# Kernel optimization log

Hardware: AMD Instinct MI355X
Metric: run time of the kernel (lower is better)

Reference implementation:

```python
import jax, jax.numpy as jnp
import numpy as np

B, T, C, H = 4, 2048, 1024, 16
NEG = -1e9  # masked-fill value (finite to keep grads clean)


def setup_inputs() -> dict:
    key = jax.random.key(0)
    ks = jax.random.split(key, 5)
    s = 1.0 / np.sqrt(C)  # keep logits O(1) like trained linear layers
    return {
        "x": jax.random.normal(ks[0], (B, T, C), dtype=jnp.float32),
        "wq": jax.random.normal(ks[1], (C, C), dtype=jnp.float32) * s,
        "bq": jnp.zeros((C,), dtype=jnp.float32),
        "wk": jax.random.normal(ks[2], (C, C), dtype=jnp.float32) * s,
        "bk": jnp.zeros((C,), dtype=jnp.float32),
        "wv": jax.random.normal(ks[3], (C, C), dtype=jnp.float32) * s,
        "bv": jnp.zeros((C,), dtype=jnp.float32),
        "wo": jax.random.normal(ks[4], (C, C), dtype=jnp.float32) * s,
        "bo": jnp.zeros((C,), dtype=jnp.float32),
    }


def _split_heads(y):
    # [B,T,C] -> [B,H,T,hd]
    b, t, c = y.shape
    return y.reshape(b, t, H, c // H).transpose(0, 2, 1, 3)


def reference(x, wq, bq, wk, bk, wv, bv, wo, bo):
    b, t, c = x.shape
    scale = (c // H) ** (-0.5)
    q = _split_heads(x @ wq.T + bq)  # [B,H,T,hd]
    k = _split_heads(x @ wk.T + bk)
    v = _split_heads(x @ wv.T + bv)
    att = jnp.einsum("bhqd,bhkd->bhqk", q, k) * scale  # [B,H,T,T]
    causal = jnp.tril(jnp.ones((t, t), dtype=bool))
    att = jnp.where(causal[None, None], att, NEG)
    att = jax.nn.softmax(att, axis=-1)  # dropout is identity in eval mode
    y = jnp.einsum("bhqk,bhkd->bhqd", att, v)
    y = y.transpose(0, 2, 1, 3).reshape(b, t, c)
    return y @ wo.T + bo
```

## Files before the change

### kernel.cpp

```cpp
#include <hip/hip_runtime.h>


#define B_ 4
#define T_ 2048
#define C_ 1024
#define H_ 16
#define M_ 8192

typedef unsigned short u16;
typedef __bf16 bf16x8 __attribute__((ext_vector_type(8)));
typedef float f32x4 __attribute__((ext_vector_type(4)));

static __device__ __forceinline__ u16 f2bf(float f) {
  unsigned int u = __float_as_uint(f);
  u += 0x7fffu + ((u >> 16) & 1u);
  return (u16)(u >> 16);
}

static __device__ __forceinline__ void async16(const void* g, void* l) {
  __builtin_amdgcn_global_load_lds(
      (const __attribute__((address_space(1))) unsigned int*)g,
      (__attribute__((address_space(3))) unsigned int*)l, 16, 0, 0);
}

#if __has_builtin(__builtin_amdgcn_exp2f)
#define EXP2F(x) __builtin_amdgcn_exp2f(x)
#else
#define EXP2F(x) exp2f(x)
#endif

static __device__ __forceinline__ f32x4 mfma32(bf16x8 a, bf16x8 b, f32x4 c) {
  return __builtin_amdgcn_mfma_f32_16x16x32_bf16(a, b, c, 0, 0, 0);
}

#define FENCE() asm volatile("" ::: "memory")

__global__ __launch_bounds__(256) void cvt_all(const float* __restrict__ x,
                                               const float* __restrict__ w0,
                                               const float* __restrict__ w1,
                                               const float* __restrict__ w2,
                                               const float* __restrict__ w3,
                                               u16* __restrict__ xb,
                                               u16* __restrict__ wb,
                                               float s0) {
  const int NX = M_ * C_ / 4, NW = C_ * C_ / 4;
  int i = blockIdx.x * 256 + threadIdx.x;
  const float* src;
  u16* dst;
  int idx;
  float s = 1.f;
  if (i < NX) {
    src = x; dst = xb; idx = i;
  } else {
    int j = i - NX;
    int w = j / NW;
    idx = j - w * NW;
    src = (w == 0) ? w0 : (w == 1) ? w1 : (w == 2) ? w2 : w3;
    dst = wb + (size_t)w * C_ * C_;
    if (w == 0) s = s0;
  }
  float4 f = ((const float4*)src)[idx];
  ushort4 o;
  o.x = f2bf(f.x * s); o.y = f2bf(f.y * s); o.z = f2bf(f.z * s); o.w = f2bf(f.w * s);
  ((ushort4*)dst)[idx] = o;
}

__global__ __launch_bounds__(512, 2) void gemm_qkv(const u16* __restrict__ A,
                                                   const u16* __restrict__ W,
                                                   const float* __restrict__ bq,
                                                   const float* __restrict__ bk,
                                                   const float* __restrict__ bv,
                                                   float qscale,
                                                   u16* __restrict__ outqk,
                                                   u16* __restrict__ vtb) {
  __shared__ __align__(16) union {
    u16 buf[3][24576];
    u16 Cu[256 * 136];
    u16 Ct[128 * 272];
  } sm;
  const int tid = threadIdx.x, lane = tid & 63, wave = tid >> 6;
  const int quad = lane >> 4, l16 = lane & 15;
  const int wm = wave >> 1, wn = wave & 1;
  const int bid = blockIdx.x;
  const int xcd = bid & 7, idx = bid >> 3;
  const int cq = idx >> 2;
  const int row0 = (xcd * 4 + (idx & 3)) * 256;
  const int sel = cq >> 3, colw = cq & 7;
  const int col0 = colw * 128;
  const u16* Bt = W + (size_t)sel * C_ * C_;
  const float* bias = sel == 0 ? bq : (sel == 1 ? bk : bv);
  const float bscale = sel == 0 ? qscale : 1.f;

  const u16* aptr[4];
  const u16* bptr[2];
#pragma unroll
  for (int it = 0; it < 4; it++) {
    int c = it * 512 + tid, r = c >> 3, g = (c & 7) ^ (r & 7);
    aptr[it] = A + (size_t)(row0 + r) * C_ + g * 8;
  }
#pragma unroll
  for (int it = 0; it < 2; it++) {
    int c = it * 512 + tid, r = c >> 3, g = (c & 7) ^ (r & 7);
    bptr[it] = Bt + (size_t)(col0 + r) * C_ + g * 8;
  }

  auto STAGE = [&](int t, int pp) {
    const int k0 = t * 64;
    u16* lA = sm.buf[pp];
    u16* lB = sm.buf[pp] + 16384;
#pragma unroll
    for (int it = 0; it < 4; it++)
      async16(aptr[it] + k0, lA + (size_t)(it * 512 + wave * 64) * 8);
#pragma unroll
    for (int it = 0; it < 2; it++)
      async16(bptr[it] + k0, lB + (size_t)(it * 512 + wave * 64) * 8);
  };

  f32x4 zero = {0.f, 0.f, 0.f, 0.f};
  f32x4 acc[4][4];
#pragma unroll
  for (int i = 0; i < 4; i++)
#pragma unroll
    for (int j = 0; j < 4; j++) acc[i][j] = zero;

  STAGE(0, 0);
  STAGE(1, 1);

  int p = 0, p2 = 2;
#pragma unroll 1
  for (int u = 0; u < 16; ++u) {
    FENCE();
    __builtin_amdgcn_s_barrier();
    FENCE();
    if (u < 14) STAGE(u + 2, p2);
    if (u < 14) {
      asm volatile("s_waitcnt vmcnt(12)" ::: "memory");
    } else if (u < 15) {
      asm volatile("s_waitcnt vmcnt(6)" ::: "memory");
    } else {
      asm volatile("s_waitcnt vmcnt(0)" ::: "memory");
    }
    FENCE();
    __builtin_amdgcn_s_barrier();
    FENCE();

    const u16* As = sm.buf[p];
    const u16* Bs = sm.buf[p] + 16384;
    bf16x8 bfr[4][2];
#pragma unroll
    for (int j = 0; j < 4; j++) {
      int rn = wn * 64 + 16 * j + l16;
#pragma unroll
      for (int kk = 0; kk < 2; kk++)
        bfr[j][kk] =
            *(const bf16x8*)(Bs + rn * 64 + (((kk * 4 + quad) ^ (rn & 7)) * 8));
    }
    {
      bf16x8 a2[2][2];
#pragma unroll
      for (int i = 0; i < 2; i++) {
        int rm = wm * 64 + 16 * i + l16;
#pragma unroll
        for (int kk = 0; kk < 2; kk++)
          a2[i][kk] =
              *(const bf16x8*)(As + rm * 64 + (((kk * 4 + quad) ^ (rm & 7)) * 8));
      }
      __builtin_amdgcn_s_setprio(1);
#pragma unroll
      for (int i = 0; i < 2; i++)
#pragma unroll
        for (int j = 0; j < 4; j++) {
          acc[i][j] = mfma32(a2[i][0], bfr[j][0], acc[i][j]);
          acc[i][j] = mfma32(a2[i][1], bfr[j][1], acc[i][j]);
        }
      __builtin_amdgcn_s_setprio(0);
    }
    FENCE();
    __builtin_amdgcn_s_barrier();
    FENCE();
    {
      bf16x8 a2[2][2];
#pragma unroll
      for (int i = 0; i < 2; i++) {
        int rm = wm * 64 + 16 * (i + 2) + l16;
#pragma unroll
        for (int kk = 0; kk < 2; kk++)
          a2[i][kk] =
              *(const bf16x8*)(As + rm * 64 + (((kk * 4 + quad) ^ (rm & 7)) * 8));
      }
      __builtin_amdgcn_s_setprio(1);
#pragma unroll
      for (int i = 0; i < 2; i++)
#pragma unroll
        for (int j = 0; j < 4; j++) {
          acc[i + 2][j] = mfma32(a2[i][0], bfr[j][0], acc[i + 2][j]);
          acc[i + 2][j] = mfma32(a2[i][1], bfr[j][1], acc[i + 2][j]);
        }
      __builtin_amdgcn_s_setprio(0);
    }
    asm volatile("s_waitcnt lgkmcnt(0)" ::: "memory");
    p = (p == 2) ? 0 : p + 1;
    p2 = (p2 == 2) ? 0 : p2 + 1;
  }
  __syncthreads();

  float bj[4];
#pragma unroll
  for (int j = 0; j < 4; j++) bj[j] = bias[col0 + wn * 64 + 16 * j + l16] * bscale;

  if (sel == 2) {
#pragma unroll
    for (int i = 0; i < 4; i++)
#pragma unroll
      for (int j = 0; j < 4; j++) {
        int lc = wn * 64 + 16 * j + l16;
        int rt = wm * 64 + 16 * i + quad * 4;
        union { u16 s[4]; uint2 u; } w;
#pragma unroll
        for (int r = 0; r < 4; r++) w.s[r] = f2bf(acc[i][j][r] + bj[j]);
        *(uint2*)(sm.Ct + (size_t)lc * 272 + rt) = w.u;
      }
    __syncthreads();
    const int bb = row0 >> 11, t0 = row0 & 2047;
#pragma unroll
    for (int c2 = 0; c2 < 8; c2++) {
      int c = c2 * 512 + tid;
      int nr = c >> 5, ch = c & 31;
      bf16x8 v = *(const bf16x8*)(sm.Ct + (size_t)nr * 272 + ch * 8);
      int gn = col0 + nr, d = gn & 63, hh = gn >> 6;
      *(bf16x8*)(vtb + ((size_t)((bb * 16 + hh) * 64 + d)) * T_ + t0 + ch * 8) = v;
    }
  } else {
#pragma unroll
    for (int i = 0; i < 4; i++)
#pragma unroll
      for (int j = 0; j < 4; j++) {
        int lc = wn * 64 + 16 * j + l16;
        int rt = wm * 64 + 16 * i + quad * 4;
#pragma unroll
        for (int r = 0; r < 4; r++)
          sm.Cu[(size_t)(rt + r) * 136 + lc] = f2bf(acc[i][j][r] + bj[j]);
      }
    __syncthreads();
    u16* dst = outqk + (size_t)sel * M_ * C_;
#pragma unroll
    for (int c2 = 0; c2 < 8; c2++) {
      int c = c2 * 512 + tid;
      int rw = c >> 4, ch = c & 15;
      bf16x8 v = *(const bf16x8*)(sm.Cu + (size_t)rw * 136 + ch * 8);
      *(bf16x8*)(dst + (size_t)(row0 + rw) * C_ + col0 + ch * 8) = v;
    }
  }
}

__global__ __launch_bounds__(512, 2) void gemm_o(const u16* __restrict__ A,
                                                 const u16* __restrict__ Bt,
                                                 const float* __restrict__ bias,
                                                 float* __restrict__ outf) {
  __shared__ __align__(16) union {
    u16 buf[3][24576];
    float Cf[256 * 132];
  } sm;
  const int tid = threadIdx.x, lane = tid & 63, wave = tid >> 6;
  const int quad = lane >> 4, l16 = lane & 15;
  const int wm = wave >> 1, wn = wave & 1;
  const int bid = blockIdx.x;
  const int xcd = bid & 7, idx = bid >> 3;
  const int row0 = (xcd * 4 + (idx & 3)) * 256;
  const int col0 = (idx >> 2) * 128;

  const u16* aptr[4];
  const u16* bptr[2];
#pragma unroll
  for (int it = 0; it < 4; it++) {
    int c = it * 512 + tid, r = c >> 3, g = (c & 7) ^ (r & 7);
    aptr[it] = A + (size_t)(row0 + r) * C_ + g * 8;
  }
#pragma unroll
  for (int it = 0; it < 2; it++) {
    int c = it * 512 + tid, r = c >> 3, g = (c & 7) ^ (r & 7);
    bptr[it] = Bt + (size_t)(col0 + r) * C_ + g * 8;
  }

  auto STAGE = [&](int t, int pp) {
    const int k0 = t * 64;
    u16* lA = sm.buf[pp];
    u16* lB = sm.buf[pp] + 16384;
#pragma unroll
    for (int it = 0; it < 4; it++)
      async16(aptr[it] + k0, lA + (size_t)(it * 512 + wave * 64) * 8);
#pragma unroll
    for (int it = 0; it < 2; it++)
      async16(bptr[it] + k0, lB + (size_t)(it * 512 + wave * 64) * 8);
  };

  f32x4 zero = {0.f, 0.f, 0.f, 0.f};
  f32x4 acc[4][4];
#pragma unroll
  for (int i = 0; i < 4; i++)
#pragma unroll
    for (int j = 0; j < 4; j++) acc[i][j] = zero;

  STAGE(0, 0);
  STAGE(1, 1);

  int p = 0, p2 = 2;
#pragma unroll 1
  for (int u = 0; u < 16; ++u) {
    FENCE();
    __builtin_amdgcn_s_barrier();
    FENCE();
    if (u < 14) STAGE(u + 2, p2);
    if (u < 14) {
      asm volatile("s_waitcnt vmcnt(12)" ::: "memory");
    } else if (u < 15) {
      asm volatile("s_waitcnt vmcnt(6)" ::: "memory");
    } else {
      asm volatile("s_waitcnt vmcnt(0)" ::: "memory");
    }
    FENCE();
    __builtin_amdgcn_s_barrier();
    FENCE();

    const u16* As = sm.buf[p];
    const u16* Bs = sm.buf[p] + 16384;
    bf16x8 bfr[4][2];
#pragma unroll
    for (int j = 0; j < 4; j++) {
      int rn = wn * 64 + 16 * j + l16;
#pragma unroll
      for (int kk = 0; kk < 2; kk++)
        bfr[j][kk] =
            *(const bf16x8*)(Bs + rn * 64 + (((kk * 4 + quad) ^ (rn & 7)) * 8));
    }
    {
      bf16x8 a2[2][2];
#pragma unroll
      for (int i = 0; i < 2; i++) {
        int rm = wm * 64 + 16 * i + l16;
#pragma unroll
        for (int kk = 0; kk < 2; kk++)
          a2[i][kk] =
              *(const bf16x8*)(As + rm * 64 + (((kk * 4 + quad) ^ (rm & 7)) * 8));
      }
      __builtin_amdgcn_s_setprio(1);
#pragma unroll
      for (int i = 0; i < 2; i++)
#pragma unroll
        for (int j = 0; j < 4; j++) {
          acc[i][j] = mfma32(a2[i][0], bfr[j][0], acc[i][j]);
          acc[i][j] = mfma32(a2[i][1], bfr[j][1], acc[i][j]);
        }
      __builtin_amdgcn_s_setprio(0);
    }
    FENCE();
    __builtin_amdgcn_s_barrier();
    FENCE();
    {
      bf16x8 a2[2][2];
#pragma unroll
      for (int i = 0; i < 2; i++) {
        int rm = wm * 64 + 16 * (i + 2) + l16;
#pragma unroll
        for (int kk = 0; kk < 2; kk++)
          a2[i][kk] =
              *(const bf16x8*)(As + rm * 64 + (((kk * 4 + quad) ^ (rm & 7)) * 8));
      }
      __builtin_amdgcn_s_setprio(1);
#pragma unroll
      for (int i = 0; i < 2; i++)
#pragma unroll
        for (int j = 0; j < 4; j++) {
          acc[i + 2][j] = mfma32(a2[i][0], bfr[j][0], acc[i + 2][j]);
          acc[i + 2][j] = mfma32(a2[i][1], bfr[j][1], acc[i + 2][j]);
        }
      __builtin_amdgcn_s_setprio(0);
    }
    asm volatile("s_waitcnt lgkmcnt(0)" ::: "memory");
    p = (p == 2) ? 0 : p + 1;
    p2 = (p2 == 2) ? 0 : p2 + 1;
  }
  __syncthreads();

  float bj[4];
#pragma unroll
  for (int j = 0; j < 4; j++) bj[j] = bias[col0 + wn * 64 + 16 * j + l16];

#pragma unroll
  for (int i = 0; i < 4; i++)
#pragma unroll
    for (int j = 0; j < 4; j++) {
      int lc = wn * 64 + 16 * j + l16;
      int rt = wm * 64 + 16 * i + quad * 4;
#pragma unroll
      for (int r = 0; r < 4; r++)
        sm.Cf[(size_t)(rt + r) * 132 + lc] = acc[i][j][r] + bj[j];
    }
  __syncthreads();
#pragma unroll
  for (int c2 = 0; c2 < 16; c2++) {
    int c = c2 * 512 + tid;
    int rw = c >> 5, c4 = c & 31;
    float4 v = *(const float4*)(sm.Cf + (size_t)rw * 132 + c4 * 4);
    *(float4*)(outf + (size_t)(row0 + rw) * C_ + col0 + c4 * 4) = v;
  }
}

__global__ __launch_bounds__(256) void attn(const u16* __restrict__ q,
                                            const u16* __restrict__ k,
                                            const u16* __restrict__ vt,
                                            u16* __restrict__ y) {
  __shared__ __align__(16) u16 Ksm[128 * 64];
  __shared__ __align__(16) u16 Vsm[2][64 * 64];
  __shared__ __align__(16) u16 Psm[4][32 * 64];
  const int tid = threadIdx.x, lane = tid & 63, wave = tid >> 6;
  const int quad = lane >> 4, l16 = lane & 15;
  static const int qperm[16] = {15, 14, 11, 10, 12, 13, 8, 9, 3, 2, 7, 6, 0, 1, 4, 5};
  const int bh = blockIdx.x;
  const int qt = qperm[blockIdx.y];
  const int b = bh >> 4, h = bh & 15;

  bf16x8 qf[2][2];
#pragma unroll
  for (int m = 0; m < 2; m++) {
    const u16* qp =
        q + (size_t)(b * T_ + qt * 128 + wave * 32 + m * 16 + l16) * C_ + h * 64;
#pragma unroll
    for (int ks = 0; ks < 2; ks++)
      qf[m][ks] = *(const bf16x8*)(qp + ks * 32 + quad * 8);
  }

  f32x4 zero = {0.f, 0.f, 0.f, 0.f};
  f32x4 o[2][4];
  float lp[2][4];
#pragma unroll
  for (int m = 0; m < 2; m++) {
#pragma unroll
    for (int dt = 0; dt < 4; dt++) o[m][dt] = zero;
#pragma unroll
    for (int r = 0; r < 4; r++) lp[m][r] = 0.f;
  }

  const u16* kp[4];
  const u16* vp[4];
#pragma unroll
  for (int i = 0; i < 4; i++) {
    int c = i * 256 + tid;
    int r = c >> 3, lc = (c & 7) ^ (r & 7);
    kp[i] = k + (size_t)(b * T_ + r) * C_ + h * 64 + lc * 8;
  }
#pragma unroll
  for (int s = 0; s < 2; s++)
#pragma unroll
    for (int i = 0; i < 2; i++) {
      int c = i * 256 + tid;
      int r = c >> 3, lc = (c & 7) ^ (r & 7);
      vp[s * 2 + i] = vt + (size_t)(bh * 64 + r) * T_ + 64 * s + lc * 8;
    }

  int qrel[2];
#pragma unroll
  for (int m = 0; m < 2; m++)
    qrel[m] = wave * 32 + m * 16 + quad * 4 - l16;

  u16* Pw = &Psm[wave][0];

#pragma unroll 1
  for (int jt = 0; jt <= qt; ++jt) {
#pragma unroll
    for (int i = 0; i < 4; i++) {
      async16(kp[i], Ksm + (size_t)(i * 256 + wave * 64) * 8);
      kp[i] += (size_t)128 * C_;
    }
#pragma unroll
    for (int s = 0; s < 2; s++)
#pragma unroll
      for (int i = 0; i < 2; i++) {
        async16(vp[s * 2 + i], Vsm[s] + (size_t)(i * 256 + wave * 64) * 8);
        vp[s * 2 + i] += 128;
      }
    __syncthreads();

    const bool diag = (jt == qt);
#pragma unroll
    for (int hh = 0; hh < 2; ++hh) {
      if (diag && (2 * wave + 2 - 4 * hh) <= 0) continue;
#pragma unroll
      for (int n = 0; n < 4; ++n) {
        int rk = hh * 64 + n * 16 + l16;
        bf16x8 kf0 = *(const bf16x8*)(Ksm + rk * 64 + ((quad ^ (rk & 7)) * 8));
        bf16x8 kf1 = *(const bf16x8*)(Ksm + rk * 64 + (((4 + quad) ^ (rk & 7)) * 8));
#pragma unroll
        for (int m = 0; m < 2; ++m) {
          int nlim = diag ? (2 * wave + m + 1 - 4 * hh) : 4;
          if (n < nlim) {
            f32x4 s = mfma32(qf[m][0], kf0, zero);
            s = mfma32(qf[m][1], kf1, s);
            float e[4];
#pragma unroll
            for (int r = 0; r < 4; r++) e[r] = EXP2F(s[r]);
            if (diag) {
              int rmin = hh * 64 + n * 16 - qrel[m];
#pragma unroll
              for (int r = 0; r < 4; r++)
                if (r < rmin) e[r] = 0.f;
            }
#pragma unroll
            for (int r = 0; r < 4; r++) {
              lp[m][r] += e[r];
              int qr = m * 16 + quad * 4 + r;
              Pw[qr * 64 + (((n * 2 + (l16 >> 3)) ^ (qr & 7)) * 8) + (l16 & 7)] =
                  f2bf(e[r]);
            }
          } else {
#pragma unroll
            for (int r = 0; r < 4; r++) {
              int qr = m * 16 + quad * 4 + r;
              Pw[qr * 64 + (((n * 2 + (l16 >> 3)) ^ (qr & 7)) * 8) + (l16 & 7)] = 0;
            }
          }
        }
      }
      bf16x8 pf[2][2];
#pragma unroll
      for (int m = 0; m < 2; m++)
#pragma unroll
        for (int ks = 0; ks < 2; ks++)
          pf[m][ks] = *(const bf16x8*)(Pw + (m * 16 + l16) * 64 +
                                       (((ks * 4 + quad) ^ (l16 & 7)) * 8));
#pragma unroll
      for (int dt = 0; dt < 4; ++dt) {
        int rv = dt * 16 + l16;
        bf16x8 vf0 = *(const bf16x8*)(Vsm[hh] + rv * 64 + ((quad ^ (rv & 7)) * 8));
        bf16x8 vf1 = *(const bf16x8*)(Vsm[hh] + rv * 64 + (((4 + quad) ^ (rv & 7)) * 8));
#pragma unroll
        for (int m = 0; m < 2; m++) {
          o[m][dt] = mfma32(pf[m][0], vf0, o[m][dt]);
          o[m][dt] = mfma32(pf[m][1], vf1, o[m][dt]);
        }
      }
    }
    __syncthreads();
  }

#pragma unroll
  for (int m = 0; m < 2; m++)
#pragma unroll
    for (int r = 0; r < 4; r++) {
      float v = lp[m][r];
      v += __shfl_xor(v, 1);
      v += __shfl_xor(v, 2);
      v += __shfl_xor(v, 4);
      v += __shfl_xor(v, 8);
      lp[m][r] = 1.f / v;
    }

#pragma unroll
  for (int m = 0; m < 2; m++)
#pragma unroll
    for (int r = 0; r < 4; r++) {
      int grow = b * T_ + qt * 128 + wave * 32 + m * 16 + quad * 4 + r;
#pragma unroll
      for (int dt = 0; dt < 4; dt++)
        y[(size_t)grow * C_ + h * 64 + dt * 16 + l16] = f2bf(o[m][dt][r] * lp[m][r]);
    }
}

extern "C" void kernel_launch(void* const* d_in, const int* in_sizes, int n_in,
                              void* d_out, int out_size, void* d_ws, size_t ws_size,
                              hipStream_t stream) {
  const float* x  = (const float*)d_in[0];
  const float* wq = (const float*)d_in[1];
  const float* bq = (const float*)d_in[2];
  const float* wk = (const float*)d_in[3];
  const float* bk = (const float*)d_in[4];
  const float* wv = (const float*)d_in[5];
  const float* bv = (const float*)d_in[6];
  const float* wo = (const float*)d_in[7];
  const float* bo = (const float*)d_in[8];
  float* out = (float*)d_out;

  const float QSCALE = 0.125f * 1.4426950408889634f;

  u16* xb  = (u16*)d_ws;
  u16* wqb = xb  + (size_t)M_ * C_;
  u16* wob = wqb + 3 * (size_t)C_ * C_;
  u16* qb  = wob + (size_t)C_ * C_;
  u16* kb  = qb  + (size_t)M_ * C_;
  u16* vtb = kb  + (size_t)M_ * C_;
  u16* yb  = xb;

  const int NCVT = (M_ * C_ + 4 * C_ * C_) / 4 / 256;
  cvt_all<<<NCVT, 256, 0, stream>>>(x, wq, wk, wv, wo, xb, wqb, QSCALE);

  gemm_qkv<<<768, 512, 0, stream>>>(xb, wqb, bq, bk, bv, QSCALE, qb, vtb);

  attn<<<dim3(B_ * H_, 16), 256, 0, stream>>>(qb, kb, vtb, yb);

  gemm_o<<<256, 512, 0, stream>>>(yb, wob, bo, out);
}
```

Before: 263.1 us.

## Transpose QK^T MFMA output in attention for vectorized P stores and cheaper row sums

Swaps the MFMA operand order so each lane holds four consecutive key columns of one query row. P can then be written to LDS as a single 4-element bf16 vector instead of four scalar stores, and row sums are kept per lane and reduced with two shuffles instead of sixteen. The causal mask condition is reworked to match the new orientation, and the final normalizer is gathered per row with a shuffle. Launch bounds for both GEMM kernels also drop from 2 to 1 blocks per CU, which frees registers but may reduce occupancy.

New measurement: 256.0 us. 1.03x faster.

```diff
diff --git a/kernel.cpp b/kernel.cpp
--- a/kernel.cpp
+++ b/kernel.cpp
@@ -9,6 +9,7 @@
 
 typedef unsigned short u16;
 typedef __bf16 bf16x8 __attribute__((ext_vector_type(8)));
+typedef __bf16 bf16x4 __attribute__((ext_vector_type(4)));
 typedef float f32x4 __attribute__((ext_vector_type(4)));
 
 static __device__ __forceinline__ u16 f2bf(float f) {
@@ -65,7 +66,7 @@
   ((ushort4*)dst)[idx] = o;
 }
 
-__global__ __launch_bounds__(512, 2) void gemm_qkv(const u16* __restrict__ A,
+__global__ __launch_bounds__(512, 1) void gemm_qkv(const u16* __restrict__ A,
                                                    const u16* __restrict__ W,
                                                    const float* __restrict__ bq,
                                                    const float* __restrict__ bk,
@@ -253,7 +254,7 @@
   }
 }
 
-__global__ __launch_bounds__(512, 2) void gemm_o(const u16* __restrict__ A,
+__global__ __launch_bounds__(512, 1) void gemm_o(const u16* __restrict__ A,
                                                  const u16* __restrict__ Bt,
                                                  const float* __restrict__ bias,
                                                  float* __restrict__ outf) {
@@ -432,14 +433,11 @@
 
   f32x4 zero = {0.f, 0.f, 0.f, 0.f};
   f32x4 o[2][4];
-  float lp[2][4];
-#pragma unroll
-  for (int m = 0; m < 2; m++) {
+  float lps[2] = {0.f, 0.f};
+#pragma unroll
+  for (int m = 0; m < 2; m++)
 #pragma unroll
     for (int dt = 0; dt < 4; dt++) o[m][dt] = zero;
-#pragma unroll
-    for (int r = 0; r < 4; r++) lp[m][r] = 0.f;
-  }
 
   const u16* kp[4];
   const u16* vp[4];
@@ -458,11 +456,7 @@
       vp[s * 2 + i] = vt + (size_t)(bh * 64 + r) * T_ + 64 * s + lc * 8;
     }
 
-  int qrel[2];
-#pragma unroll
-  for (int m = 0; m < 2; m++)
-    qrel[m] = wave * 32 + m * 16 + quad * 4 - l16;
-
+  const int qrow = wave * 32 + l16;
   u16* Pw = &Psm[wave][0];
 
 #pragma unroll 1
@@ -493,31 +487,30 @@
 #pragma unroll
         for (int m = 0; m < 2; ++m) {
           int nlim = diag ? (2 * wave + m + 1 - 4 * hh) : 4;
+          int qr = m * 16 + l16;
+          int off = qr * 64 + (((n * 2 + (quad >> 1)) ^ (qr & 7)) * 8) + (quad & 1) * 4;
           if (n < nlim) {
-            f32x4 s = mfma32(qf[m][0], kf0, zero);
-            s = mfma32(qf[m][1], kf1, s);
+            f32x4 s = mfma32(kf0, qf[m][0], zero);
+            s = mfma32(kf1, qf[m][1], s);
             float e[4];
 #pragma unroll
             for (int r = 0; r < 4; r++) e[r] = EXP2F(s[r]);
             if (diag) {
-              int rmin = hh * 64 + n * 16 - qrel[m];
+              int rmax = qrow + m * 16 - hh * 64 - n * 16 - quad * 4;
 #pragma unroll
               for (int r = 0; r < 4; r++)
-                if (r < rmin) e[r] = 0.f;
+                if (r > rmax) e[r] = 0.f;
             }
-#pragma unroll
-            for (int r = 0; r < 4; r++) {
-              lp[m][r] += e[r];
-              int qr = m * 16 + quad * 4 + r;
-              Pw[qr * 64 + (((n * 2 + (l16 >> 3)) ^ (qr & 7)) * 8) + (l16 & 7)] =
-                  f2bf(e[r]);
-            }
+            lps[m] += (e[0] + e[1]) + (e[2] + e[3]);
+            bf16x4 pw;
+#pragma unroll
+            for (int r = 0; r < 4; r++) pw[r] = (__bf16)e[r];
+            *(bf16x4*)(Pw + off) = pw;
           } else {
-#pragma unroll
-            for (int r = 0; r < 4; r++) {
-              int qr = m * 16 + quad * 4 + r;
-              Pw[qr * 64 + (((n * 2 + (l16 >> 3)) ^ (qr & 7)) * 8) + (l16 & 7)] = 0;
-            }
+            bf16x4 z;
+#pragma unroll
+            for (int r = 0; r < 4; r++) z[r] = (__bf16)0.f;
+            *(bf16x4*)(Pw + off) = z;
           }
         }
       }
@@ -543,26 +536,24 @@
     __syncthreads();
   }
 
+  float linv[2];
+#pragma unroll
+  for (int m = 0; m < 2; m++) {
+    float v = lps[m];
+    v += __shfl_xor(v, 16);
+    v += __shfl_xor(v, 32);
+    linv[m] = 1.f / v;
+  }
+
 #pragma unroll
   for (int m = 0; m < 2; m++)
 #pragma unroll
     for (int r = 0; r < 4; r++) {
-      float v = lp[m][r];
-      v += __shfl_xor(v, 1);
-      v += __shfl_xor(v, 2);
-      v += __shfl_xor(v, 4);
-      v += __shfl_xor(v, 8);
-      lp[m][r] = 1.f / v;
-    }
-
-#pragma unroll
-  for (int m = 0; m < 2; m++)
-#pragma unroll
-    for (int r = 0; r < 4; r++) {
+      float il = __shfl(linv[m], quad * 4 + r);
       int grow = b * T_ + qt * 128 + wave * 32 + m * 16 + quad * 4 + r;
 #pragma unroll
       for (int dt = 0; dt < 4; dt++)
-        y[(size_t)grow * C_ + h * 64 + dt * 16 + l16] = f2bf(o[m][dt][r] * lp[m][r]);
+        y[(size_t)grow * C_ + h * 64 + dt * 16 + l16] = f2bf(o[m][dt][r] * il);
     }
 }
 
```
